# Kernel tuning notes

Hardware: AMD Instinct MI355X
Metric: run time of the kernel (lower is better)

The kernel has to match this reference:

```python
import jax, jax.numpy as jnp
import numpy as np

T, B, D, H = 2048, 2, 1024, 16
NH, DH = H // 2, D // H   # 8 heads per direction, d_head = 64
DFF = 4096


def layer_norm(x, g, b, eps=1e-5):
    mu = jnp.mean(x, axis=-1, keepdims=True)
    var = jnp.mean(jnp.square(x - mu), axis=-1, keepdims=True)
    return (x - mu) * jax.lax.rsqrt(var + eps) * g + b


def rel_shift(x):
    # x: [q, k, b, n] -> Transformer-XL relative shift
    q, k, b, n = x.shape
    x = jnp.concatenate([jnp.zeros((q, 1, b, n), x.dtype), x], axis=1)
    return x.reshape(k + 1, q, b, n)[1:].reshape(q, k, b, n)


def rel_attn(w, r, mask, qkv_w, r_w, r_w_bias, r_r_bias):
    # w: [T, B, D], r: [R, 1, D], mask: [T, T] bool (True = masked)
    t, b, _ = w.shape
    heads = jnp.einsum('tbd,ed->tbe', w, qkv_w)              # [T,B,3*NH*DH]
    q, k, v = jnp.split(heads, 3, axis=-1)
    q = q.reshape(t, b, NH, DH)
    k = k.reshape(t, b, NH, DH)
    v = v.reshape(t, b, NH, DH)
    rk = jnp.einsum('rd,ed->re', r[:, 0, :], r_w).reshape(-1, NH, DH)  # [R,NH,DH]
    AC = jnp.einsum('ibnd,jbnd->ijbn', q + r_w_bias, k)
    BD = rel_shift(jnp.einsum('ibnd,jnd->ijbn', q + r_r_bias, rk))
    score = (AC + BD) * (1.0 / np.sqrt(DH))
    score = jnp.where(mask[:, :, None, None], jnp.finfo(score.dtype).min, score)
    prob = jax.nn.softmax(score, axis=1)
    vec = jnp.einsum('ijbn,jbnd->ibnd', prob, v)
    return vec.reshape(t, b, NH * DH)


def setup_inputs() -> dict:
    key = jax.random.key(0)
    ks = jax.random.split(key, 24)
    s = 0.02
    causal = jnp.triu(jnp.ones((T, T), dtype=bool), k=1)
    return {
        'x': jax.random.normal(ks[0], (T, B, D), jnp.float32),
        'pos': jax.random.normal(ks[1], (T, 1, D), jnp.float32),
        'mask_fwd': causal,
        'mask_bwd': causal,
        'ln1_g': jnp.ones((D,), jnp.float32), 'ln1_b': jnp.zeros((D,), jnp.float32),
        'ln2_g': jnp.ones((D,), jnp.float32), 'ln2_b': jnp.zeros((D,), jnp.float32),
        'ln3_g': jnp.ones((D,), jnp.float32), 'ln3_b': jnp.zeros((D,), jnp.float32),
        'qkv_f': jax.random.normal(ks[2], (3 * NH * DH, D), jnp.float32) * s,
        'rnet_f': jax.random.normal(ks[3], (NH * DH, D), jnp.float32) * s,
        'rwb_f': jax.random.normal(ks[4], (NH, DH), jnp.float32) * s,
        'rrb_f': jax.random.normal(ks[5], (NH, DH), jnp.float32) * s,
        'qkv_b': jax.random.normal(ks[6], (3 * NH * DH, D), jnp.float32) * s,
        'rnet_b': jax.random.normal(ks[7], (NH * DH, D), jnp.float32) * s,
        'rwb_b': jax.random.normal(ks[8], (NH, DH), jnp.float32) * s,
        'rrb_b': jax.random.normal(ks[9], (NH, DH), jnp.float32) * s,
        'wo': jax.random.normal(ks[10], (D, D), jnp.float32) * s,
        'bo': jnp.zeros((D,), jnp.float32),
        'w1': jax.random.normal(ks[11], (DFF, D), jnp.float32) * s,
        'b1': jnp.zeros((DFF,), jnp.float32),
        'w2': jax.random.normal(ks[12], (D, DFF), jnp.float32) * s,
        'b2': jnp.zeros((D,), jnp.float32),
    }


def reference(x, pos, mask_fwd, mask_bwd,
              ln1_g, ln1_b, ln2_g, ln2_b, ln3_g, ln3_b,
              qkv_f, rnet_f, rwb_f, rrb_f,
              qkv_b, rnet_b, rwb_b, rrb_b,
              wo, bo, w1, b1, w2, b2):
    # --- bidirectional relative attention ---
    q_fwd = layer_norm(x, ln1_g, ln1_b)
    q_bwd = layer_norm(jnp.flip(x, axis=0), ln2_g, ln2_b)
    out_fwd = rel_attn(q_fwd, pos, mask_fwd, qkv_f, rnet_f, rwb_f, rrb_f)
    out_bwd = rel_attn(q_bwd, pos, mask_bwd, qkv_b, rnet_b, rwb_b, rrb_b)
    out = jnp.concatenate([out_fwd, jnp.flip(out_bwd, axis=0)], axis=-1)
    out = jnp.einsum('tbd,ed->tbe', out, wo) + bo
    h = x + out                     # postprocess_attn: dropout(id) + residual
    # --- feed forward: LN -> Linear -> ReLU -> Linear -> residual ---
    y = layer_norm(h, ln3_g, ln3_b)
    y = jax.nn.relu(jnp.einsum('tbd,fd->tbf', y, w1) + b1)
    y = jnp.einsum('tbf,df->tbd', y, w2) + b2
    return h + y
```

## Files before the change

### kernel.cpp

```cpp
#include <hip/hip_runtime.h>
#include <cstdint>
#include <cstddef>


typedef unsigned short ushort_t;
typedef __bf16 bf16x8 __attribute__((ext_vector_type(8)));
typedef float f32x4 __attribute__((ext_vector_type(4)));
typedef unsigned short us8 __attribute__((ext_vector_type(8)));
typedef unsigned short us4 __attribute__((ext_vector_type(4)));

#define DEV static __device__ __forceinline__

DEV ushort_t f2bf(float x) {
  union { float f; unsigned u; } v; v.f = x;
  unsigned r = (v.u + 0x7FFFu + ((v.u >> 16) & 1u)) >> 16;
  return (ushort_t)r;
}
DEV ushort_t f2bt(float x) {
  union { float f; unsigned u; } v; v.f = x;
  return (ushort_t)(v.u >> 16);
}
DEV float bf2f(ushort_t h) {
  union { unsigned u; float f; } v; v.u = ((unsigned)h) << 16;
  return v.f;
}
DEV float fexp2(float x) { float r; asm("v_exp_f32 %0, %1" : "=v"(r) : "v"(x)); return r; }
DEV f32x4 mfma16(bf16x8 a, bf16x8 b, f32x4 c) {
  return __builtin_amdgcn_mfma_f32_16x16x32_bf16(a, b, c, 0, 0, 0);
}
DEV void gld16(const void* g, void* l) {
  __builtin_amdgcn_global_load_lds((const __attribute__((address_space(1))) void*)g,
                                   (__attribute__((address_space(3))) void*)l,
                                   16, 0, 0);
}

constexpr size_t O_QKV_F  = 0;
constexpr size_t O_QKV_B  = 3145728;
constexpr size_t O_RNET_F = 6291456;
constexpr size_t O_RNET_B = 7340032;
constexpr size_t O_WO     = 8388608;
constexpr size_t O_W1     = 10485760;
constexpr size_t O_W2     = 18874368;
constexpr size_t O_RKREV_F= 27262976;
constexpr size_t O_RKREV_B= 29360128;
constexpr size_t O_QAC_F  = 31457280;
constexpr size_t O_QBD_F  = 35651584;
constexpr size_t O_KK_F   = 39845888;
constexpr size_t O_VT_F   = 44040192;
constexpr size_t O_QAC_B  = 48234496;
constexpr size_t O_QBD_B  = 52428800;
constexpr size_t O_KK_B   = 56623104;
constexpr size_t O_VT_B   = 60817408;
constexpr size_t O_H      = 65011712;
constexpr size_t O_LN3    = 81788928;
constexpr size_t ZONE     = 90177536;
constexpr size_t O_POS    = ZONE + 0;
constexpr size_t O_LN1    = ZONE + 4194304;
constexpr size_t O_LN2    = ZONE + 12582912;
constexpr size_t O_HEADS_F= ZONE + 20971520;
constexpr size_t O_HEADS_B= ZONE + 33554432;
constexpr size_t O_ACAT   = ZONE + 0;
constexpr size_t O_FFNM   = ZONE + 8388608;

struct CvtArgs {
  const float* src[8];
  ushort_t* dst[8];
  int bstart[8];
};
__global__ __launch_bounds__(256)
void cvt_all_k(CvtArgs a) {
  int bx = blockIdx.x;
  int s = 0;
#pragma unroll
  for (int k = 1; k < 8; ++k) if (bx >= a.bstart[k]) s = k;
  int i = (bx - a.bstart[s]) * 256 + threadIdx.x;
  float4 v = reinterpret_cast<const float4*>(a.src[s])[i];
  us4 o; o[0] = f2bf(v.x); o[1] = f2bf(v.y); o[2] = f2bf(v.z); o[3] = f2bf(v.w);
  reinterpret_cast<us4*>(a.dst[s])[i] = o;
}

__global__ __launch_bounds__(256)
void ln_dual_k(const float* __restrict__ x,
               const float* __restrict__ g1, const float* __restrict__ b1,
               const float* __restrict__ g2, const float* __restrict__ b2,
               ushort_t* __restrict__ o1, ushort_t* __restrict__ o2) {
  __shared__ float sbuf[8];
  const int row = blockIdx.x;
  const int tid = threadIdx.x;
  const float* xr = x + (size_t)row * 1024;
  float4 v = reinterpret_cast<const float4*>(xr)[tid];
  float s  = v.x + v.y + v.z + v.w;
  float s2 = v.x*v.x + v.y*v.y + v.z*v.z + v.w*v.w;
  for (int m = 32; m >= 1; m >>= 1) { s += __shfl_xor(s, m, 64); s2 += __shfl_xor(s2, m, 64); }
  int w = tid >> 6;
  if ((tid & 63) == 0) { sbuf[w] = s; sbuf[4 + w] = s2; }
  __syncthreads();
  float S  = sbuf[0] + sbuf[1] + sbuf[2] + sbuf[3];
  float S2 = sbuf[4] + sbuf[5] + sbuf[6] + sbuf[7];
  float mu  = S * (1.f / 1024.f);
  float var = S2 * (1.f / 1024.f) - mu * mu;
  float inv = rsqrtf(var + 1e-5f);
  int t = row >> 1, b = row & 1;
  size_t r2 = ((size_t)(2047 - t) * 2 + b) * 1024;
  float4 G1 = reinterpret_cast<const float4*>(g1)[tid];
  float4 B1 = reinterpret_cast<const float4*>(b1)[tid];
  float4 G2 = reinterpret_cast<const float4*>(g2)[tid];
  float4 B2 = reinterpret_cast<const float4*>(b2)[tid];
  float n0 = (v.x - mu) * inv, n1 = (v.y - mu) * inv, n2 = (v.z - mu) * inv, n3 = (v.w - mu) * inv;
  us4 a, c;
  a[0] = f2bf(n0 * G1.x + B1.x); a[1] = f2bf(n1 * G1.y + B1.y);
  a[2] = f2bf(n2 * G1.z + B1.z); a[3] = f2bf(n3 * G1.w + B1.w);
  c[0] = f2bf(n0 * G2.x + B2.x); c[1] = f2bf(n1 * G2.y + B2.y);
  c[2] = f2bf(n2 * G2.z + B2.z); c[3] = f2bf(n3 * G2.w + B2.w);
  reinterpret_cast<us4*>(o1 + (size_t)row * 1024)[tid] = a;
  reinterpret_cast<us4*>(o2 + r2)[tid] = c;
}

__global__ __launch_bounds__(256)
void ln_one_k(const float* __restrict__ x,
              const float* __restrict__ g1, const float* __restrict__ b1,
              ushort_t* __restrict__ o1) {
  __shared__ float sbuf[8];
  const int row = blockIdx.x;
  const int tid = threadIdx.x;
  const float* xr = x + (size_t)row * 1024;
  float4 v = reinterpret_cast<const float4*>(xr)[tid];
  float s  = v.x + v.y + v.z + v.w;
  float s2 = v.x*v.x + v.y*v.y + v.z*v.z + v.w*v.w;
  for (int m = 32; m >= 1; m >>= 1) { s += __shfl_xor(s, m, 64); s2 += __shfl_xor(s2, m, 64); }
  int w = tid >> 6;
  if ((tid & 63) == 0) { sbuf[w] = s; sbuf[4 + w] = s2; }
  __syncthreads();
  float S  = sbuf[0] + sbuf[1] + sbuf[2] + sbuf[3];
  float S2 = sbuf[4] + sbuf[5] + sbuf[6] + sbuf[7];
  float mu  = S * (1.f / 1024.f);
  float var = S2 * (1.f / 1024.f) - mu * mu;
  float inv = rsqrtf(var + 1e-5f);
  float4 G1 = reinterpret_cast<const float4*>(g1)[tid];
  float4 B1 = reinterpret_cast<const float4*>(b1)[tid];
  us4 a;
  a[0] = f2bf((v.x - mu) * inv * G1.x + B1.x);
  a[1] = f2bf((v.y - mu) * inv * G1.y + B1.y);
  a[2] = f2bf((v.z - mu) * inv * G1.z + B1.z);
  a[3] = f2bf((v.w - mu) * inv * G1.w + B1.w);
  reinterpret_cast<us4*>(o1 + (size_t)row * 1024)[tid] = a;
}

template <int EPI>
__global__ __launch_bounds__(256)
void gemm_bt(const ushort_t* __restrict__ A, const ushort_t* __restrict__ B,
             void* __restrict__ C, const float* __restrict__ bias,
             const float* __restrict__ resid, int M, int N, int K) {
  __shared__ ushort_t As[128 * 64];
  __shared__ ushort_t Bs[128 * 64];
  const int tid = threadIdx.x;
  const int lane = tid & 63;
  const int w = tid >> 6;
  const int wm = w >> 1, wn = w & 1;
  const int row0 = blockIdx.y * 128, col0 = blockIdx.x * 128;
  const int lr = lane & 15;
  const int lkb = (lane >> 4) * 8;
  const int rr = lane >> 3;
  const int scb = ((lane & 7) ^ rr) * 8;
  const f32x4 fz = {0.f, 0.f, 0.f, 0.f};
  f32x4 acc[4][4];
#pragma unroll
  for (int i = 0; i < 4; ++i)
#pragma unroll
    for (int j = 0; j < 4; ++j) acc[i][j] = fz;

  for (int k0 = 0; k0 < K; k0 += 64) {
    __syncthreads();
#pragma unroll
    for (int it = 0; it < 4; ++it) {
      int rbase = it * 32 + w * 8;
      gld16(A + (size_t)(row0 + rbase + rr) * K + k0 + scb, (char*)As + rbase * 128);
      gld16(B + (size_t)(col0 + rbase + rr) * K + k0 + scb, (char*)Bs + rbase * 128);
    }
    __syncthreads();
#pragma unroll
    for (int kk = 0; kk < 64; kk += 32) {
      bf16x8 af[4], bfr[4];
#pragma unroll
      for (int mi = 0; mi < 4; ++mi) {
        int r = wm * 64 + mi * 16 + lr;
        int off = (r * 128 + (kk + lkb) * 2) ^ ((r & 7) << 4);
        af[mi] = *reinterpret_cast<const bf16x8*>((char*)As + off);
      }
#pragma unroll
      for (int ni = 0; ni < 4; ++ni) {
        int r = wn * 64 + ni * 16 + lr;
        int off = (r * 128 + (kk + lkb) * 2) ^ ((r & 7) << 4);
        bfr[ni] = *reinterpret_cast<const bf16x8*>((char*)Bs + off);
      }
#pragma unroll
      for (int mi = 0; mi < 4; ++mi)
#pragma unroll
        for (int ni = 0; ni < 4; ++ni)
          acc[mi][ni] = mfma16(af[mi], bfr[ni], acc[mi][ni]);
    }
  }
#pragma unroll
  for (int mi = 0; mi < 4; ++mi)
#pragma unroll
    for (int ni = 0; ni < 4; ++ni)
#pragma unroll
      for (int r = 0; r < 4; ++r) {
        int row = row0 + wm * 64 + mi * 16 + (lane >> 4) * 4 + r;
        int col = col0 + wn * 64 + ni * 16 + lr;
        float v = acc[mi][ni][r];
        if (EPI == 0) {
          ((ushort_t*)C)[(size_t)row * N + col] = f2bf(v);
        } else if (EPI == 1) {
          v += bias[col]; v = v > 0.f ? v : 0.f;
          ((ushort_t*)C)[(size_t)row * N + col] = f2bf(v);
        } else {
          v += bias[col] + resid[(size_t)row * N + col];
          ((float*)C)[(size_t)row * N + col] = v;
        }
      }
}

template <int EPI>
__global__ __launch_bounds__(256)
void gemm64(const ushort_t* __restrict__ A0, const ushort_t* __restrict__ A1,
            const ushort_t* __restrict__ B0, const ushort_t* __restrict__ B1,
            void* __restrict__ C0, void* __restrict__ C1,
            const float* __restrict__ bias, const float* __restrict__ resid,
            int M, int N, int K) {
  __shared__ ushort_t As[64 * 64];
  __shared__ ushort_t Bs[128 * 64];
  const ushort_t* A = blockIdx.z ? A1 : A0;
  const ushort_t* B = blockIdx.z ? B1 : B0;
  void* C = blockIdx.z ? (void*)C1 : (void*)C0;
  const int tid = threadIdx.x;
  const int lane = tid & 63;
  const int w = tid >> 6;
  const int wm = w >> 1, wn = w & 1;
  const int row0 = blockIdx.y * 64, col0 = blockIdx.x * 128;
  const int lr = lane & 15;
  const int lkb = (lane >> 4) * 8;
  const int rr = lane >> 3;
  const int scb = ((lane & 7) ^ rr) * 8;
  const f32x4 fz = {0.f, 0.f, 0.f, 0.f};
  f32x4 acc[2][4];
#pragma unroll
  for (int i = 0; i < 2; ++i)
#pragma unroll
    for (int j = 0; j < 4; ++j) acc[i][j] = fz;

  for (int k0 = 0; k0 < K; k0 += 64) {
    __syncthreads();
#pragma unroll
    for (int it = 0; it < 2; ++it) {
      int rbase = it * 32 + w * 8;
      gld16(A + (size_t)(row0 + rbase + rr) * K + k0 + scb, (char*)As + rbase * 128);
    }
#pragma unroll
    for (int it = 0; it < 4; ++it) {
      int rbase = it * 32 + w * 8;
      gld16(B + (size_t)(col0 + rbase + rr) * K + k0 + scb, (char*)Bs + rbase * 128);
    }
    __syncthreads();
#pragma unroll
    for (int kk = 0; kk < 64; kk += 32) {
      bf16x8 af[2], bfr[4];
#pragma unroll
      for (int mi = 0; mi < 2; ++mi) {
        int r = wm * 32 + mi * 16 + lr;
        int off = (r * 128 + (kk + lkb) * 2) ^ ((r & 7) << 4);
        af[mi] = *reinterpret_cast<const bf16x8*>((char*)As + off);
      }
#pragma unroll
      for (int ni = 0; ni < 4; ++ni) {
        int r = wn * 64 + ni * 16 + lr;
        int off = (r * 128 + (kk + lkb) * 2) ^ ((r & 7) << 4);
        bfr[ni] = *reinterpret_cast<const bf16x8*>((char*)Bs + off);
      }
#pragma unroll
      for (int mi = 0; mi < 2; ++mi)
#pragma unroll
        for (int ni = 0; ni < 4; ++ni)
          acc[mi][ni] = mfma16(af[mi], bfr[ni], acc[mi][ni]);
    }
  }
#pragma unroll
  for (int mi = 0; mi < 2; ++mi)
#pragma unroll
    for (int ni = 0; ni < 4; ++ni)
#pragma unroll
      for (int r = 0; r < 4; ++r) {
        int row = row0 + wm * 32 + mi * 16 + (lane >> 4) * 4 + r;
        int col = col0 + wn * 64 + ni * 16 + lr;
        float v = acc[mi][ni][r];
        if (EPI == 0) {
          ((ushort_t*)C)[(size_t)row * N + col] = f2bf(v);
        } else if (EPI == 1) {
          v += bias[col]; v = v > 0.f ? v : 0.f;
          ((ushort_t*)C)[(size_t)row * N + col] = f2bf(v);
        } else if (EPI == 2) {
          v += bias[col] + resid[(size_t)row * N + col];
          ((float*)C)[(size_t)row * N + col] = v;
        } else {
          int nn = col >> 6, dh = col & 63;
          ((ushort_t*)C)[((size_t)nn * 2048 + (2047 - row)) * 64 + dh] = f2bf(v);
        }
      }
}

__global__ __launch_bounds__(256)
void qkv_post2_k(const ushort_t* __restrict__ hf, const ushort_t* __restrict__ hb2,
                 const float* __restrict__ rwf, const float* __restrict__ rrf,
                 const float* __restrict__ rwb2, const float* __restrict__ rrb2,
                 char* __restrict__ wsb) {
  const float SCL = 0.125f * 1.44269504088896f;
  const int dir = blockIdx.y;
  const ushort_t* heads = dir ? hb2 : hf;
  const float* rwb = dir ? rwb2 : rwf;
  const float* rrb = dir ? rrb2 : rrf;
  ushort_t* q_ac = (ushort_t*)(wsb + (dir ? O_QAC_B : O_QAC_F));
  ushort_t* q_bd = (ushort_t*)(wsb + (dir ? O_QBD_B : O_QBD_F));
  ushort_t* kout = (ushort_t*)(wsb + (dir ? O_KK_B : O_KK_F));
  int row = blockIdx.x;
  int t = row >> 1, b = row & 1;
#pragma unroll
  for (int c0 = 0; c0 < 1024; c0 += 256) {
    int c = c0 + threadIdx.x;
    ushort_t hv = heads[(size_t)row * 1536 + c];
    if (c < 512) {
      int n = c >> 6, dh = c & 63;
      size_t o = ((size_t)(b * 8 + n) * 2048 + t) * 64 + dh;
      float q = bf2f(hv);
      q_ac[o] = f2bf((q + rwb[c]) * SCL);
      q_bd[o] = f2bf((q + rrb[c]) * SCL);
    } else {
      int cc = c - 512;
      int n = cc >> 6, dh = cc & 63;
      kout[((size_t)(b * 8 + n) * 2048 + t) * 64 + dh] = hv;
    }
  }
}

__global__ __launch_bounds__(256)
void v_trans2_k(const ushort_t* __restrict__ hf, const ushort_t* __restrict__ hb2,
                char* __restrict__ wsb) {
  __shared__ float tile[64][65];
  const int dir = blockIdx.z;
  const ushort_t* heads = dir ? hb2 : hf;
  ushort_t* vt = (ushort_t*)(wsb + (dir ? O_VT_B : O_VT_F));
  int tt0 = blockIdx.x * 64;
  int bn = blockIdx.y;
  int b = bn >> 3, n = bn & 7;
  int tid = threadIdx.x;
#pragma unroll
  for (int i = 0; i < 16; ++i) {
    int rr = i * 4 + (tid >> 6);
    int cc = tid & 63;
    tile[rr][cc] = bf2f(heads[(size_t)((tt0 + rr) * 2 + b) * 1536 + 1024 + n * 64 + cc]);
  }
  __syncthreads();
#pragma unroll
  for (int i = 0; i < 16; ++i) {
    int dh = i * 4 + (tid >> 6);
    int tt = tid & 63;
    vt[((size_t)bn * 64 + dh) * 2048 + tt0 + tt] = f2bf(tile[tt][dh]);
  }
}

__global__ __launch_bounds__(256)
void attn_k(const char* __restrict__ wsb, ushort_t* __restrict__ outp) {
  __shared__ ushort_t Kbuf[2][64 * 64];
  __shared__ ushort_t Vbuf[2][64 * 64];
  __shared__ ushort_t Gs[4][16 * 84];
  __shared__ ushort_t Ps[4][1024];

  const int tid = threadIdx.x;
  const int lane = tid & 63;
  const int w = tid >> 6;
  const int il = lane & 15;
  const int g = lane >> 4;
  const int lkb = g * 8;
  const int rr = lane >> 3;
  const int scb = ((lane & 7) ^ rr) * 8;

  const int id = (int)(blockIdx.x + (blockIdx.y << 4) + (blockIdx.z << 8));
  const int xcd = id & 7;
  const int ord = id >> 3;
  const int pair = xcd * 4 + (ord & 3);
  const int bx = ord >> 2;
  const int bn = pair & 15;
  const int dir = pair >> 4;

  const ushort_t* qac  = (const ushort_t*)(wsb + (dir ? O_QAC_B : O_QAC_F));
  const ushort_t* qbd  = (const ushort_t*)(wsb + (dir ? O_QBD_B : O_QBD_F));
  const ushort_t* kkv  = (const ushort_t*)(wsb + (dir ? O_KK_B  : O_KK_F));
  const ushort_t* vtp  = (const ushort_t*)(wsb + (dir ? O_VT_B  : O_VT_F));
  const ushort_t* rkrev= (const ushort_t*)(wsb + (dir ? O_RKREV_B : O_RKREV_F));
  const int colbase = dir ? 512 : 0;

  const size_t hb = (size_t)bn * 2048;
  const size_t vbase = (size_t)bn * 64;
  const size_t nb = (size_t)(bn & 7) * 2048;
  const int b = bn >> 3;
  const int n = bn & 7;

  ushort_t* gw = Gs[w];
  char* pw = (char*)Ps[w];

  for (int half = 0; half < 2; ++half) {
    const int it = half ? bx : (31 - bx);
    const int i0 = it * 64;
    const int NT = it + 1;
    const int iw0 = i0 + w * 16;

    auto STAGE = [&](int bi, int j0) {
      ushort_t* kb = Kbuf[bi] + w * 512;
      ushort_t* vbp = Vbuf[bi] + w * 512;
      gld16(kkv + (hb + j0 + w * 8 + rr) * 64 + scb, kb);
      gld16(kkv + (hb + j0 + 32 + w * 8 + rr) * 64 + scb, kb + 2048);
      gld16(vtp + (vbase + w * 8 + rr) * 2048 + j0 + scb, vbp);
      gld16(vtp + (vbase + 32 + w * 8 + rr) * 2048 + j0 + scb, vbp + 2048);
    };

    bf16x8 qa[2], qb[2];
#pragma unroll
    for (int kf = 0; kf < 2; ++kf) {
      size_t off = (hb + iw0 + il) * 64 + kf * 32 + lkb;
      qa[kf] = *reinterpret_cast<const bf16x8*>(qac + off);
      qb[kf] = *reinterpret_cast<const bf16x8*>(qbd + off);
    }

    const f32x4 fz = {0.f, 0.f, 0.f, 0.f};
    f32x4 Oa[4];
#pragma unroll
    for (int nf = 0; nf < 4; ++nf) Oa[nf] = fz;
    float lsum = 0.f;

    STAGE(0, 0);
    __syncthreads();
    int cur = 0;
    for (int jt = 0; jt < NT; ++jt) {
      const int j0 = jt * 64;

      bf16x8 bd0[5], bd1[5];
      const int dbase = iw0 - j0 - 63;
#pragma unroll
      for (int ng = 0; ng < 5; ++ng) {
        int d = dbase + ng * 16 + il;
        d = d < 0 ? 0 : (d > 2047 ? 2047 : d);
        const ushort_t* bp = rkrev + (nb + d) * 64 + lkb;
        bd0[ng] = *reinterpret_cast<const bf16x8*>(bp);
        bd1[ng] = *reinterpret_cast<const bf16x8*>(bp + 32);
      }
      if (jt + 1 < NT) STAGE(cur ^ 1, j0 + 64);

      const ushort_t* Ks = Kbuf[cur];
      const ushort_t* Vs = Vbuf[cur];
      f32x4 S[4], G[5];
#pragma unroll
      for (int nf = 0; nf < 4; ++nf) S[nf] = fz;
#pragma unroll
      for (int ng = 0; ng < 5; ++ng) G[ng] = fz;
      __builtin_amdgcn_s_setprio(1);
#pragma unroll
      for (int kf = 0; kf < 2; ++kf)
#pragma unroll
        for (int nf = 0; nf < 4; ++nf) {
          int r = nf * 16 + il;
          int off = (r * 128 + (kf * 32 + lkb) * 2) ^ ((r & 7) << 4);
          S[nf] = mfma16(*reinterpret_cast<const bf16x8*>((char*)Ks + off), qa[kf], S[nf]);
        }
#pragma unroll
      for (int ng = 0; ng < 5; ++ng) {
        G[ng] = mfma16(bd0[ng], qb[0], G[ng]);
        G[ng] = mfma16(bd1[ng], qb[1], G[ng]);
      }
      __builtin_amdgcn_s_setprio(0);
#pragma unroll
      for (int ng = 0; ng < 5; ++ng) {
        us4 pk;
        pk[0] = f2bt(G[ng][0]); pk[1] = f2bt(G[ng][1]);
        pk[2] = f2bt(G[ng][2]); pk[3] = f2bt(G[ng][3]);
        *reinterpret_cast<us4*>(gw + il * 84 + ng * 16 + g * 4) = pk;
      }
      asm volatile("s_waitcnt lgkmcnt(0)" ::: "memory");
      const bool full = (j0 + 63 <= iw0);
#pragma unroll
      for (int nf = 0; nf < 4; ++nf)
#pragma unroll
        for (int r = 0; r < 4; ++r) {
          int jl = nf * 16 + g * 4 + r;
          float sv = S[nf][r] + bf2f(gw[il * 84 + (il - jl + 63)]);
          if (!full) sv = (j0 + jl <= iw0 + il) ? sv : -1e30f;
          S[nf][r] = sv;
        }
#pragma unroll
      for (int nf = 0; nf < 4; ++nf) {
        us4 pk;
#pragma unroll
        for (int r = 0; r < 4; ++r) {
          float p = fexp2(S[nf][r]);
          lsum += p;
          pk[r] = f2bt(p);
        }
        int off = (il * 128 + (nf * 16 + g * 4) * 2) ^ ((il & 7) << 4);
        *reinterpret_cast<us4*>(pw + off) = pk;
      }
      asm volatile("s_waitcnt lgkmcnt(0)" ::: "memory");
      __builtin_amdgcn_s_setprio(1);
#pragma unroll
      for (int kf = 0; kf < 2; ++kf) {
        int poff = (il * 128 + (kf * 32 + lkb) * 2) ^ ((il & 7) << 4);
        bf16x8 pt = *reinterpret_cast<const bf16x8*>(pw + poff);
#pragma unroll
        for (int nf = 0; nf < 4; ++nf) {
          int r = nf * 16 + il;
          int voff = (r * 128 + (kf * 32 + lkb) * 2) ^ ((r & 7) << 4);
          Oa[nf] = mfma16(*reinterpret_cast<const bf16x8*>((char*)Vs + voff), pt, Oa[nf]);
        }
      }
      __builtin_amdgcn_s_setprio(0);
      __syncthreads();
      cur ^= 1;
    }
    lsum += __shfl_xor(lsum, 16, 64);
    lsum += __shfl_xor(lsum, 32, 64);
    float invl = 1.f / lsum;
    int ig = iw0 + il;
    int tout = dir ? (2047 - ig) : ig;
    size_t orow = ((size_t)tout * 2 + b) * 1024 + colbase + n * 64;
#pragma unroll
    for (int nf = 0; nf < 4; ++nf) {
      us4 pk;
#pragma unroll
      for (int r = 0; r < 4; ++r) pk[r] = f2bf(Oa[nf][r] * invl);
      *reinterpret_cast<us4*>(outp + orow + nf * 16 + g * 4) = pk;
    }
    lsum = 0.f;
  }
}

extern "C" void kernel_launch(void* const* d_in, const int* in_sizes, int n_in,
                              void* d_out, int out_size, void* d_ws, size_t ws_size,
                              hipStream_t stream) {
  (void)in_sizes; (void)n_in; (void)out_size; (void)ws_size;
  const float* x    = (const float*)d_in[0];
  const float* pos  = (const float*)d_in[1];
  const float* ln1g = (const float*)d_in[4];
  const float* ln1b = (const float*)d_in[5];
  const float* ln2g = (const float*)d_in[6];
  const float* ln2b = (const float*)d_in[7];
  const float* ln3g = (const float*)d_in[8];
  const float* ln3b = (const float*)d_in[9];
  const float* qkvf = (const float*)d_in[10];
  const float* rnetf= (const float*)d_in[11];
  const float* rwbf = (const float*)d_in[12];
  const float* rrbf = (const float*)d_in[13];
  const float* qkvb = (const float*)d_in[14];
  const float* rnetb= (const float*)d_in[15];
  const float* rwbb = (const float*)d_in[16];
  const float* rrbb = (const float*)d_in[17];
  const float* wo   = (const float*)d_in[18];
  const float* bo   = (const float*)d_in[19];
  const float* w1   = (const float*)d_in[20];
  const float* b1   = (const float*)d_in[21];
  const float* w2   = (const float*)d_in[22];
  const float* b2   = (const float*)d_in[23];
  float* out = (float*)d_out;
  char* ws = (char*)d_ws;
  auto U = [&](size_t off) { return (ushort_t*)(ws + off); };

  CvtArgs ca;
  const float* srcs[8] = {qkvf, qkvb, rnetf, rnetb, wo, w1, w2, pos};
  size_t dsts[8] = {O_QKV_F, O_QKV_B, O_RNET_F, O_RNET_B, O_WO, O_W1, O_W2, O_POS};
  int bl[8] = {1536, 1536, 512, 512, 1024, 4096, 4096, 2048};
  int cum = 0;
  for (int s = 0; s < 8; ++s) {
    ca.src[s] = srcs[s];
    ca.dst[s] = U(dsts[s]);
    ca.bstart[s] = cum;
    cum += bl[s];
  }
  cvt_all_k<<<dim3(cum), dim3(256), 0, stream>>>(ca);

  ln_dual_k<<<dim3(4096), dim3(256), 0, stream>>>(x, ln1g, ln1b, ln2g, ln2b, U(O_LN1), U(O_LN2));

  gemm64<0><<<dim3(12, 64, 2), dim3(256), 0, stream>>>(
      U(O_LN1), U(O_LN2), U(O_QKV_F), U(O_QKV_B), U(O_HEADS_F), U(O_HEADS_B),
      nullptr, nullptr, 4096, 1536, 1024);
  gemm64<3><<<dim3(4, 32, 2), dim3(256), 0, stream>>>(
      U(O_POS), U(O_POS), U(O_RNET_F), U(O_RNET_B), U(O_RKREV_F), U(O_RKREV_B),
      nullptr, nullptr, 2048, 512, 1024);

  qkv_post2_k<<<dim3(4096, 2), dim3(256), 0, stream>>>(
      U(O_HEADS_F), U(O_HEADS_B), rwbf, rrbf, rwbb, rrbb, ws);
  v_trans2_k<<<dim3(32, 16, 2), dim3(256), 0, stream>>>(U(O_HEADS_F), U(O_HEADS_B), ws);

  attn_k<<<dim3(16, 16, 2), dim3(256), 0, stream>>>(ws, U(O_ACAT));

  gemm64<2><<<dim3(8, 64, 1), dim3(256), 0, stream>>>(
      U(O_ACAT), U(O_ACAT), U(O_WO), U(O_WO), ws + O_H, ws + O_H,
      bo, x, 4096, 1024, 1024);

  ln_one_k<<<dim3(4096), dim3(256), 0, stream>>>((const float*)(ws + O_H), ln3g, ln3b, U(O_LN3));
  gemm_bt<1><<<dim3(32, 32), dim3(256), 0, stream>>>(U(O_LN3), U(O_W1), U(O_FFNM), b1, nullptr, 4096, 4096, 1024);
  gemm64<2><<<dim3(8, 64, 1), dim3(256), 0, stream>>>(
      U(O_FFNM), U(O_FFNM), U(O_W2), U(O_W2), out, out,
      b2, (const float*)(ws + O_H), 4096, 1024, 4096);
}
```

Before: 342.7 us.

## Switch attention to 32x32 MFMA with 128-row query tiles and register P exchange

Rewrites the attention kernel to use 32x32x16 bf16 MFMA instructions, giving each wave 32 query rows and each block one 128-row tile instead of two paired 64-row tiles. The P matrix is now passed between lanes with cross-lane shuffles instead of a round trip through shared memory, and the relative-position G tile is read with packed 64-bit loads. Waves whose rows lie entirely above the causal diagonal skip compute but still issue staging loads. The changes are meant to reduce LDS traffic and instruction count per FLOP. In exchange, load balance across blocks changes, and the larger accumulators raise register pressure under the new launch bound of 2.

```diff
diff --git a/kernel.cpp b/kernel.cpp
--- a/kernel.cpp
+++ b/kernel.cpp
@@ -6,6 +6,7 @@
 typedef unsigned short ushort_t;
 typedef __bf16 bf16x8 __attribute__((ext_vector_type(8)));
 typedef float f32x4 __attribute__((ext_vector_type(4)));
+typedef float f32x16 __attribute__((ext_vector_type(16)));
 typedef unsigned short us8 __attribute__((ext_vector_type(8)));
 typedef unsigned short us4 __attribute__((ext_vector_type(4)));
 
@@ -27,6 +28,9 @@
 DEV float fexp2(float x) { float r; asm("v_exp_f32 %0, %1" : "=v"(r) : "v"(x)); return r; }
 DEV f32x4 mfma16(bf16x8 a, bf16x8 b, f32x4 c) {
   return __builtin_amdgcn_mfma_f32_16x16x32_bf16(a, b, c, 0, 0, 0);
+}
+DEV f32x16 mfma32(bf16x8 a, bf16x8 b, f32x16 c) {
+  return __builtin_amdgcn_mfma_f32_32x32x16_bf16(a, b, c, 0, 0, 0);
 }
 DEV void gld16(const void* g, void* l) {
   __builtin_amdgcn_global_load_lds((const __attribute__((address_space(1))) void*)g,
@@ -367,19 +371,17 @@
   }
 }
 
-__global__ __launch_bounds__(256)
+__global__ __launch_bounds__(256, 2)
 void attn_k(const char* __restrict__ wsb, ushort_t* __restrict__ outp) {
   __shared__ ushort_t Kbuf[2][64 * 64];
   __shared__ ushort_t Vbuf[2][64 * 64];
-  __shared__ ushort_t Gs[4][16 * 84];
-  __shared__ ushort_t Ps[4][1024];
+  __shared__ ushort_t Gs[4][32 * 100];
 
   const int tid = threadIdx.x;
   const int lane = tid & 63;
   const int w = tid >> 6;
-  const int il = lane & 15;
-  const int g = lane >> 4;
-  const int lkb = g * 8;
+  const int il = lane & 31;
+  const int hi = lane >> 5;
   const int rr = lane >> 3;
   const int scb = ((lane & 7) ^ rr) * 8;
 
@@ -387,7 +389,7 @@
   const int xcd = id & 7;
   const int ord = id >> 3;
   const int pair = xcd * 4 + (ord & 3);
-  const int bx = ord >> 2;
+  const int it = 15 - (ord >> 2);
   const int bn = pair & 15;
   const int dir = pair >> 4;
 
@@ -405,139 +407,160 @@
   const int n = bn & 7;
 
   ushort_t* gw = Gs[w];
-  char* pw = (char*)Ps[w];
-
-  for (int half = 0; half < 2; ++half) {
-    const int it = half ? bx : (31 - bx);
-    const int i0 = it * 64;
-    const int NT = it + 1;
-    const int iw0 = i0 + w * 16;
-
-    auto STAGE = [&](int bi, int j0) {
-      ushort_t* kb = Kbuf[bi] + w * 512;
-      ushort_t* vbp = Vbuf[bi] + w * 512;
-      gld16(kkv + (hb + j0 + w * 8 + rr) * 64 + scb, kb);
-      gld16(kkv + (hb + j0 + 32 + w * 8 + rr) * 64 + scb, kb + 2048);
-      gld16(vtp + (vbase + w * 8 + rr) * 2048 + j0 + scb, vbp);
-      gld16(vtp + (vbase + 32 + w * 8 + rr) * 2048 + j0 + scb, vbp + 2048);
-    };
-
-    bf16x8 qa[2], qb[2];
-#pragma unroll
-    for (int kf = 0; kf < 2; ++kf) {
-      size_t off = (hb + iw0 + il) * 64 + kf * 32 + lkb;
-      qa[kf] = *reinterpret_cast<const bf16x8*>(qac + off);
-      qb[kf] = *reinterpret_cast<const bf16x8*>(qbd + off);
-    }
-
-    const f32x4 fz = {0.f, 0.f, 0.f, 0.f};
-    f32x4 Oa[4];
-#pragma unroll
-    for (int nf = 0; nf < 4; ++nf) Oa[nf] = fz;
-    float lsum = 0.f;
-
-    STAGE(0, 0);
-    __syncthreads();
-    int cur = 0;
-    for (int jt = 0; jt < NT; ++jt) {
-      const int j0 = jt * 64;
-
-      bf16x8 bd0[5], bd1[5];
+
+  const int i0 = it * 128;
+  const int NT = 2 * it + 2;
+  const int iw0 = i0 + w * 32;
+
+  auto STAGE = [&](int bi, int j0) {
+    ushort_t* kb = Kbuf[bi] + w * 512;
+    ushort_t* vbp = Vbuf[bi] + w * 512;
+    gld16(kkv + (hb + j0 + w * 8 + rr) * 64 + scb, kb);
+    gld16(kkv + (hb + j0 + 32 + w * 8 + rr) * 64 + scb, kb + 2048);
+    gld16(vtp + (vbase + w * 8 + rr) * 2048 + j0 + scb, vbp);
+    gld16(vtp + (vbase + 32 + w * 8 + rr) * 2048 + j0 + scb, vbp + 2048);
+  };
+
+  bf16x8 qa[4], qb[4];
+#pragma unroll
+  for (int kf = 0; kf < 4; ++kf) {
+    size_t off = (hb + iw0 + il) * 64 + kf * 16 + hi * 8;
+    qa[kf] = *reinterpret_cast<const bf16x8*>(qac + off);
+    qb[kf] = *reinterpret_cast<const bf16x8*>(qbd + off);
+  }
+
+  f32x16 Oa[2];
+#pragma unroll
+  for (int dhf = 0; dhf < 2; ++dhf)
+#pragma unroll
+    for (int e = 0; e < 16; ++e) Oa[dhf][e] = 0.f;
+  float lsum = 0.f;
+
+  STAGE(0, 0);
+  __syncthreads();
+  int cur = 0;
+  for (int jt = 0; jt < NT; ++jt) {
+    const int j0 = jt * 64;
+    const bool active = (j0 <= iw0 + 31);
+
+    if (active) {
+      bf16x8 bd[3][4];
       const int dbase = iw0 - j0 - 63;
 #pragma unroll
-      for (int ng = 0; ng < 5; ++ng) {
-        int d = dbase + ng * 16 + il;
+      for (int cf = 0; cf < 3; ++cf) {
+        int d = dbase + cf * 32 + il;
         d = d < 0 ? 0 : (d > 2047 ? 2047 : d);
-        const ushort_t* bp = rkrev + (nb + d) * 64 + lkb;
-        bd0[ng] = *reinterpret_cast<const bf16x8*>(bp);
-        bd1[ng] = *reinterpret_cast<const bf16x8*>(bp + 32);
+        const ushort_t* bp = rkrev + (nb + d) * 64 + hi * 8;
+#pragma unroll
+        for (int kf = 0; kf < 4; ++kf)
+          bd[cf][kf] = *reinterpret_cast<const bf16x8*>(bp + kf * 16);
       }
       if (jt + 1 < NT) STAGE(cur ^ 1, j0 + 64);
 
       const ushort_t* Ks = Kbuf[cur];
       const ushort_t* Vs = Vbuf[cur];
-      f32x4 S[4], G[5];
-#pragma unroll
-      for (int nf = 0; nf < 4; ++nf) S[nf] = fz;
-#pragma unroll
-      for (int ng = 0; ng < 5; ++ng) G[ng] = fz;
-      __builtin_amdgcn_s_setprio(1);
-#pragma unroll
-      for (int kf = 0; kf < 2; ++kf)
-#pragma unroll
-        for (int nf = 0; nf < 4; ++nf) {
-          int r = nf * 16 + il;
-          int off = (r * 128 + (kf * 32 + lkb) * 2) ^ ((r & 7) << 4);
-          S[nf] = mfma16(*reinterpret_cast<const bf16x8*>((char*)Ks + off), qa[kf], S[nf]);
+
+      f32x16 S[2];
+#pragma unroll
+      for (int jlf = 0; jlf < 2; ++jlf) {
+#pragma unroll
+        for (int e = 0; e < 16; ++e) S[jlf][e] = 0.f;
+        __builtin_amdgcn_s_setprio(1);
+#pragma unroll
+        for (int kf = 0; kf < 4; ++kf) {
+          int r = jlf * 32 + il;
+          int off = (r * 128 + (kf * 16 + hi * 8) * 2) ^ ((r & 7) << 4);
+          S[jlf] = mfma32(*reinterpret_cast<const bf16x8*>((char*)Ks + off), qa[kf], S[jlf]);
         }
-#pragma unroll
-      for (int ng = 0; ng < 5; ++ng) {
-        G[ng] = mfma16(bd0[ng], qb[0], G[ng]);
-        G[ng] = mfma16(bd1[ng], qb[1], G[ng]);
-      }
-      __builtin_amdgcn_s_setprio(0);
-#pragma unroll
-      for (int ng = 0; ng < 5; ++ng) {
-        us4 pk;
-        pk[0] = f2bt(G[ng][0]); pk[1] = f2bt(G[ng][1]);
-        pk[2] = f2bt(G[ng][2]); pk[3] = f2bt(G[ng][3]);
-        *reinterpret_cast<us4*>(gw + il * 84 + ng * 16 + g * 4) = pk;
+        __builtin_amdgcn_s_setprio(0);
+      }
+#pragma unroll
+      for (int cf = 0; cf < 3; ++cf) {
+        f32x16 G;
+#pragma unroll
+        for (int e = 0; e < 16; ++e) G[e] = 0.f;
+        __builtin_amdgcn_s_setprio(1);
+#pragma unroll
+        for (int kf = 0; kf < 4; ++kf) G = mfma32(bd[cf][kf], qb[kf], G);
+        __builtin_amdgcn_s_setprio(0);
+#pragma unroll
+        for (int q = 0; q < 4; ++q) {
+          us4 pk;
+          pk[0] = f2bt(G[4 * q + 0]); pk[1] = f2bt(G[4 * q + 1]);
+          pk[2] = f2bt(G[4 * q + 2]); pk[3] = f2bt(G[4 * q + 3]);
+          *reinterpret_cast<us4*>(gw + il * 100 + cf * 32 + 8 * q + 4 * hi) = pk;
+        }
       }
       asm volatile("s_waitcnt lgkmcnt(0)" ::: "memory");
-      const bool full = (j0 + 63 <= iw0);
-#pragma unroll
-      for (int nf = 0; nf < 4; ++nf)
-#pragma unroll
-        for (int r = 0; r < 4; ++r) {
-          int jl = nf * 16 + g * 4 + r;
-          float sv = S[nf][r] + bf2f(gw[il * 84 + (il - jl + 63)]);
-          if (!full) sv = (j0 + jl <= iw0 + il) ? sv : -1e30f;
-          S[nf][r] = sv;
+      const bool fullt = (j0 + 63 <= iw0);
+      unsigned pq[2][4][2];
+#pragma unroll
+      for (int jlf = 0; jlf < 2; ++jlf)
+#pragma unroll
+        for (int q = 0; q < 4; ++q) {
+          int c3 = il + 60 - jlf * 32 - 8 * q - 4 * hi;
+          int base4 = c3 & ~3;
+          int o = c3 & 3;
+          const ushort_t* gp = gw + il * 100 + base4;
+          uint64_t av = *reinterpret_cast<const uint64_t*>(gp);
+          uint64_t bv = *reinterpret_cast<const uint64_t*>(gp + 4);
+          uint64_t v = o ? ((av >> (16 * o)) | (bv << (64 - 16 * o))) : av;
+          us4 pk;
+#pragma unroll
+          for (int r = 0; r < 4; ++r) {
+            int jl = jlf * 32 + 8 * q + 4 * hi + r;
+            float sv = S[jlf][4 * q + r] + bf2f((ushort_t)(v >> (16 * (3 - r))));
+            if (!fullt) sv = (j0 + jl <= iw0 + il) ? sv : -1e30f;
+            float p = fexp2(sv);
+            lsum += p;
+            pk[r] = f2bt(p);
+          }
+          pq[jlf][q][0] = (unsigned)pk[0] | ((unsigned)pk[1] << 16);
+          pq[jlf][q][1] = (unsigned)pk[2] | ((unsigned)pk[3] << 16);
         }
 #pragma unroll
-      for (int nf = 0; nf < 4; ++nf) {
-        us4 pk;
-#pragma unroll
-        for (int r = 0; r < 4; ++r) {
-          float p = fexp2(S[nf][r]);
-          lsum += p;
-          pk[r] = f2bt(p);
+      for (int kf = 0; kf < 4; ++kf) {
+        const int jq = kf >> 1, q0 = (kf & 1) * 2, q1 = q0 + 1;
+        unsigned own0 = hi ? pq[jq][q1][0] : pq[jq][q0][0];
+        unsigned own1 = hi ? pq[jq][q1][1] : pq[jq][q0][1];
+        unsigned sd0  = hi ? pq[jq][q0][0] : pq[jq][q1][0];
+        unsigned sd1  = hi ? pq[jq][q0][1] : pq[jq][q1][1];
+        unsigned rc0 = (unsigned)__shfl_xor((int)sd0, 32, 64);
+        unsigned rc1 = (unsigned)__shfl_xor((int)sd1, 32, 64);
+        union { unsigned u[4]; bf16x8 v; } pb;
+        pb.u[0] = hi ? rc0 : own0;
+        pb.u[1] = hi ? rc1 : own1;
+        pb.u[2] = hi ? own0 : rc0;
+        pb.u[3] = hi ? own1 : rc1;
+        __builtin_amdgcn_s_setprio(1);
+#pragma unroll
+        for (int dhf = 0; dhf < 2; ++dhf) {
+          int r = dhf * 32 + il;
+          int voff = (r * 128 + (kf * 16 + hi * 8) * 2) ^ ((r & 7) << 4);
+          Oa[dhf] = mfma32(*reinterpret_cast<const bf16x8*>((char*)Vs + voff), pb.v, Oa[dhf]);
         }
-        int off = (il * 128 + (nf * 16 + g * 4) * 2) ^ ((il & 7) << 4);
-        *reinterpret_cast<us4*>(pw + off) = pk;
-      }
-      asm volatile("s_waitcnt lgkmcnt(0)" ::: "memory");
-      __builtin_amdgcn_s_setprio(1);
-#pragma unroll
-      for (int kf = 0; kf < 2; ++kf) {
-        int poff = (il * 128 + (kf * 32 + lkb) * 2) ^ ((il & 7) << 4);
-        bf16x8 pt = *reinterpret_cast<const bf16x8*>(pw + poff);
-#pragma unroll
-        for (int nf = 0; nf < 4; ++nf) {
-          int r = nf * 16 + il;
-          int voff = (r * 128 + (kf * 32 + lkb) * 2) ^ ((r & 7) << 4);
-          Oa[nf] = mfma16(*reinterpret_cast<const bf16x8*>((char*)Vs + voff), pt, Oa[nf]);
-        }
-      }
-      __builtin_amdgcn_s_setprio(0);
-      __syncthreads();
-      cur ^= 1;
-    }
-    lsum += __shfl_xor(lsum, 16, 64);
-    lsum += __shfl_xor(lsum, 32, 64);
-    float invl = 1.f / lsum;
-    int ig = iw0 + il;
-    int tout = dir ? (2047 - ig) : ig;
-    size_t orow = ((size_t)tout * 2 + b) * 1024 + colbase + n * 64;
-#pragma unroll
-    for (int nf = 0; nf < 4; ++nf) {
+        __builtin_amdgcn_s_setprio(0);
+      }
+    } else {
+      if (jt + 1 < NT) STAGE(cur ^ 1, j0 + 64);
+    }
+    __syncthreads();
+    cur ^= 1;
+  }
+  lsum += __shfl_xor(lsum, 32, 64);
+  float invl = 1.f / lsum;
+  int ig = iw0 + il;
+  int tout = dir ? (2047 - ig) : ig;
+  size_t orow = ((size_t)tout * 2 + b) * 1024 + colbase + n * 64;
+#pragma unroll
+  for (int dhf = 0; dhf < 2; ++dhf)
+#pragma unroll
+    for (int q = 0; q < 4; ++q) {
       us4 pk;
 #pragma unroll
-      for (int r = 0; r < 4; ++r) pk[r] = f2bf(Oa[nf][r] * invl);
-      *reinterpret_cast<us4*>(outp + orow + nf * 16 + g * 4) = pk;
-    }
-    lsum = 0.f;
-  }
+      for (int r = 0; r < 4; ++r) pk[r] = f2bf(Oa[dhf][4 * q + r] * invl);
+      *reinterpret_cast<us4*>(outp + orow + dhf * 32 + 8 * q + 4 * hi) = pk;
+    }
 }
 
 extern "C" void kernel_launch(void* const* d_in, const int* in_sizes, int n_in,
```

After: 355.8 us. 3.8% more time.

## Split attention key tiles across two partitions with separate reduction kernel

Applied to the files above, without the earlier changes.

The attention kernel now splits each query tile's key-tile loop into two interleaved partitions (even and odd tiles), doubling the grid so more blocks can run at once. Each partition writes unnormalized fp32 output accumulators and row sums to a workspace buffer. A new reduction kernel adds the two partials, normalizes, converts to bf16, and writes the concatenated attention output. This aims to improve occupancy and latency hiding in attention. In exchange it adds extra global memory traffic for the fp32 partials and one more kernel launch.

```diff
diff --git a/kernel.cpp b/kernel.cpp
--- a/kernel.cpp
+++ b/kernel.cpp
@@ -61,6 +61,8 @@
 constexpr size_t O_HEADS_B= ZONE + 33554432;
 constexpr size_t O_ACAT   = ZONE + 0;
 constexpr size_t O_FFNM   = ZONE + 8388608;
+constexpr size_t O_PART   = ZONE + 8388608;
+constexpr size_t O_LPART  = O_PART + 33554432;
 
 struct CvtArgs {
   const float* src[8];
@@ -368,7 +370,7 @@
 }
 
 __global__ __launch_bounds__(256)
-void attn_k(const char* __restrict__ wsb, ushort_t* __restrict__ outp) {
+void attn_k(char* __restrict__ wsb) {
   __shared__ ushort_t Kbuf[2][64 * 64];
   __shared__ ushort_t Vbuf[2][64 * 64];
   __shared__ ushort_t Gs[4][16 * 84];
@@ -383,35 +385,37 @@
   const int rr = lane >> 3;
   const int scb = ((lane & 7) ^ rr) * 8;
 
-  const int id = (int)(blockIdx.x + (blockIdx.y << 4) + (blockIdx.z << 8));
+  const int id = (int)(blockIdx.x + (blockIdx.y << 5) + (blockIdx.z << 9));
   const int xcd = id & 7;
   const int ord = id >> 3;
-  const int pair = xcd * 4 + (ord & 3);
-  const int bx = ord >> 2;
-  const int bn = pair & 15;
-  const int dir = pair >> 4;
+  const int combo = xcd * 4 + (ord & 3);
+  const int px = (ord >> 2) & 15;
+  const int par = (ord >> 6) & 1;
+  const int bn = combo & 15;
+  const int dir = combo >> 4;
 
   const ushort_t* qac  = (const ushort_t*)(wsb + (dir ? O_QAC_B : O_QAC_F));
   const ushort_t* qbd  = (const ushort_t*)(wsb + (dir ? O_QBD_B : O_QBD_F));
   const ushort_t* kkv  = (const ushort_t*)(wsb + (dir ? O_KK_B  : O_KK_F));
   const ushort_t* vtp  = (const ushort_t*)(wsb + (dir ? O_VT_B  : O_VT_F));
   const ushort_t* rkrev= (const ushort_t*)(wsb + (dir ? O_RKREV_B : O_RKREV_F));
-  const int colbase = dir ? 512 : 0;
 
   const size_t hb = (size_t)bn * 2048;
   const size_t vbase = (size_t)bn * 64;
   const size_t nb = (size_t)(bn & 7) * 2048;
-  const int b = bn >> 3;
-  const int n = bn & 7;
+
+  float* opart = (float*)(wsb + O_PART) + (((size_t)combo * 2 + par) * 2048) * 64;
+  float* lpart = (float*)(wsb + O_LPART) + ((size_t)combo * 2 + par) * 2048;
 
   ushort_t* gw = Gs[w];
   char* pw = (char*)Ps[w];
 
   for (int half = 0; half < 2; ++half) {
-    const int it = half ? bx : (31 - bx);
+    const int it = half ? px : (31 - px);
     const int i0 = it * 64;
     const int NT = it + 1;
     const int iw0 = i0 + w * 16;
+    const int first = par;
 
     auto STAGE = [&](int bi, int j0) {
       ushort_t* kb = Kbuf[bi] + w * 512;
@@ -436,10 +440,10 @@
     for (int nf = 0; nf < 4; ++nf) Oa[nf] = fz;
     float lsum = 0.f;
 
-    STAGE(0, 0);
+    if (first < NT) STAGE(0, first * 64);
     __syncthreads();
     int cur = 0;
-    for (int jt = 0; jt < NT; ++jt) {
+    for (int jt = first; jt < NT; jt += 2) {
       const int j0 = jt * 64;
 
       bf16x8 bd0[5], bd1[5];
@@ -452,7 +456,7 @@
         bd0[ng] = *reinterpret_cast<const bf16x8*>(bp);
         bd1[ng] = *reinterpret_cast<const bf16x8*>(bp + 32);
       }
-      if (jt + 1 < NT) STAGE(cur ^ 1, j0 + 64);
+      if (jt + 2 < NT) STAGE(cur ^ 1, j0 + 128);
 
       const ushort_t* Ks = Kbuf[cur];
       const ushort_t* Vs = Vbuf[cur];
@@ -525,19 +529,34 @@
     }
     lsum += __shfl_xor(lsum, 16, 64);
     lsum += __shfl_xor(lsum, 32, 64);
-    float invl = 1.f / lsum;
     int ig = iw0 + il;
-    int tout = dir ? (2047 - ig) : ig;
-    size_t orow = ((size_t)tout * 2 + b) * 1024 + colbase + n * 64;
+    float* op = opart + (size_t)ig * 64;
 #pragma unroll
     for (int nf = 0; nf < 4; ++nf) {
-      us4 pk;
-#pragma unroll
-      for (int r = 0; r < 4; ++r) pk[r] = f2bf(Oa[nf][r] * invl);
-      *reinterpret_cast<us4*>(outp + orow + nf * 16 + g * 4) = pk;
-    }
-    lsum = 0.f;
+      float4 v4 = {Oa[nf][0], Oa[nf][1], Oa[nf][2], Oa[nf][3]};
+      *reinterpret_cast<float4*>(op + nf * 16 + g * 4) = v4;
+    }
+    if (g == 0) lpart[ig] = lsum;
   }
+}
+
+__global__ __launch_bounds__(256)
+void attn_reduce_k(const char* __restrict__ wsb, ushort_t* __restrict__ outp) {
+  const int combo = blockIdx.y;
+  const int dir = combo >> 4;
+  const int bn = combo & 15;
+  const int b = bn >> 3, n = bn & 7;
+  const int colbase = dir ? 512 : 0;
+  const int rr = threadIdx.x >> 6;
+  const int dh = threadIdx.x & 63;
+  const int row = blockIdx.x * 4 + rr;
+  const float* p0 = (const float*)(wsb + O_PART) + (((size_t)combo * 2 + 0) * 2048 + row) * 64;
+  const float* p1 = p0 + (size_t)2048 * 64;
+  const float* lp = (const float*)(wsb + O_LPART) + (size_t)combo * 2 * 2048;
+  float lv = lp[row] + lp[2048 + row];
+  float o = (p0[dh] + p1[dh]) / lv;
+  int tout = dir ? (2047 - row) : row;
+  outp[((size_t)tout * 2 + b) * 1024 + colbase + n * 64 + dh] = f2bf(o);
 }
 
 extern "C" void kernel_launch(void* const* d_in, const int* in_sizes, int n_in,
@@ -596,7 +615,8 @@
       U(O_HEADS_F), U(O_HEADS_B), rwbf, rrbf, rwbb, rrbb, ws);
   v_trans2_k<<<dim3(32, 16, 2), dim3(256), 0, stream>>>(U(O_HEADS_F), U(O_HEADS_B), ws);
 
-  attn_k<<<dim3(16, 16, 2), dim3(256), 0, stream>>>(ws, U(O_ACAT));
+  attn_k<<<dim3(32, 16, 2), dim3(256), 0, stream>>>(ws);
+  attn_reduce_k<<<dim3(512, 32), dim3(256), 0, stream>>>(ws, U(O_ACAT));
 
   gemm64<2><<<dim3(8, 64, 1), dim3(256), 0, stream>>>(
       U(O_ACAT), U(O_ACAT), U(O_WO), U(O_WO), ws + O_H, ws + O_H,
```

New measurement: 371.2 us. 8.3% more time.
